# Kernel tuning notes

Measured on AMD Instinct MI355X. Metric: run time of the kernel, lower is better.

## Reference

```python
import jax, jax.numpy as jnp
import numpy as np

MAX_DISP = 4  # init kwarg


def setup_inputs() -> dict:
    key = jax.random.key(0)
    k1, k2 = jax.random.split(key)
    x_1 = jax.random.normal(k1, (8, 128, 128, 128), dtype=jnp.float32)
    x_2 = jax.random.normal(k2, (8, 128, 128, 128), dtype=jnp.float32)
    return {"x_1": x_1, "x_2": x_2}


def reference(x_1, x_2):
    d = MAX_DISP
    H, W = x_1.shape[2], x_1.shape[3]
    # zero-pad x_2 by max_disp on both spatial dims (ConstantPad2d)
    x2p = jnp.pad(x_2, ((0, 0), (0, 0), (d, d), (d, d)))
    # loop over the fixed (2d+1)^2 = 81 displacement offsets (structural, not data dim)
    outs = [
        jnp.mean(x_1 * x2p[:, :, dx:dx + H, dy:dy + W], axis=1)  # [B,H,W]
        for dx in range(2 * d + 1)
        for dy in range(2 * d + 1)
    ]
    return jnp.stack(outs, axis=1)  # [B, 81, H, W]
```

## Files before the change

kernel.cpp:

```cpp
#include <hip/hip_runtime.h>


constexpr int Cn = 128, Hn = 128, Wn = 128;
constexpr int HWn = Hn * Wn;
constexpr int TH = 4;
constexpr int NROWS = 16;
constexpr int ROWF  = 128;
constexpr int CHF   = NROWS * ROWF;
constexpr int BUFF  = 2 * CHF;

__device__ __forceinline__ float dpp_shr1(float x) {
  return __int_as_float(__builtin_amdgcn_update_dpp(
      0, __float_as_int(x), 0x111, 0xF, 0xF, true));
}
__device__ __forceinline__ float dpp_shl1(float x) {
  return __int_as_float(__builtin_amdgcn_update_dpp(
      0, __float_as_int(x), 0x101, 0xF, 0xF, true));
}

__global__ __launch_bounds__(576, 3)
void corr_kernel(const float* __restrict__ x1, const float* __restrict__ x2,
                 float* __restrict__ out) {
  __shared__ float lds[2][2][NROWS][ROWF];

  const int t    = threadIdx.x;
  const int w    = t >> 6;
  const int lane = t & 63;
  const int r    = lane >> 4;
  const int l    = lane & 15;

  const int phys = blockIdx.x;
  const int b    = phys & 7;
  const int tile = phys >> 3;
  const int h0   = tile * TH;
  const int dh   = w - 4;

  const bool stg  = t < 512;
  const int ridx  = t >> 5;
  const int s     = t & 31;
  const int j     = (s < 16) ? (s << 1) : (((s - 16) << 1) | 1);
  int gr;
  bool okg;
  if (ridx < 4) { gr = h0 + ridx; okg = true; }
  else { gr = h0 + ridx - 8; okg = (unsigned)gr < (unsigned)Hn; }
  const float* src = (ridx < 4 ? x1 : x2) + (size_t)b * Cn * HWn
                   + (size_t)(okg ? gr : 0) * Wn + (j << 2);
  okg = okg && stg;
  float* const L = &lds[0][0][0][0];
  const int woff = ridx * ROWF + (s << 2);

  const int rx  = r + dh + 8;
  const int o1l = r * ROWF + (l << 2);
  const int o1h = o1l + 64;
  const int o2l = rx * ROWF + (l << 2);
  const int o2h = o2l + 64;

  float4 acc0[9], acc1[9];
#pragma unroll
  for (int dw = 0; dw < 9; ++dw) {
    acc0[dw] = make_float4(0.f, 0.f, 0.f, 0.f);
    acc1[dw] = make_float4(0.f, 0.f, 0.f, 0.f);
  }

  const float4 z4 = make_float4(0.f, 0.f, 0.f, 0.f);
  float4 pv0 = z4, pv1 = z4;
  if (okg) { pv0 = *(const float4*)src; pv1 = *(const float4*)(src + HWn); }
  src += 2 * HWn;

#pragma unroll 1
  for (int step = 0; step < 64; ++step) {
    const int bo = (step & 1) * BUFF;
    if (stg) {
      *(float4*)(L + bo + woff)       = pv0;
      *(float4*)(L + bo + CHF + woff) = pv1;
    }
    __syncthreads();
    if (okg && step < 63) {
      pv0 = *(const float4*)src;
      pv1 = *(const float4*)(src + HWn);
    }
    src += 2 * HWn;

#pragma unroll
    for (int ch = 0; ch < 2; ++ch) {
      const float* p = L + bo + ch * CHF;
      const float4 a0 = *(const float4*)(p + o1l);
      const float4 a1 = *(const float4*)(p + o1h);
      const float4 b0 = *(const float4*)(p + o2l);
      const float4 b1 = *(const float4*)(p + o2h);
      const float win[16] = {
          dpp_shr1(b1.x), dpp_shr1(b1.y), dpp_shr1(b1.z), dpp_shr1(b1.w),
          b0.x, b0.y, b0.z, b0.w,
          b1.x, b1.y, b1.z, b1.w,
          dpp_shl1(b0.x), dpp_shl1(b0.y), dpp_shl1(b0.z), dpp_shl1(b0.w)};
      const float av[8] = {a0.x, a0.y, a0.z, a0.w, a1.x, a1.y, a1.z, a1.w};
#pragma unroll
      for (int dw = 0; dw < 9; ++dw) {
        acc0[dw].x += av[0] * win[dw + 0];
        acc0[dw].y += av[1] * win[dw + 1];
        acc0[dw].z += av[2] * win[dw + 2];
        acc0[dw].w += av[3] * win[dw + 3];
        acc1[dw].x += av[4] * win[dw + 4];
        acc1[dw].y += av[5] * win[dw + 5];
        acc1[dw].z += av[6] * win[dw + 6];
        acc1[dw].w += av[7] * win[dw + 7];
      }
    }
  }

  const float scale = 1.0f / 128.0f;
  float* ob = out + ((size_t)b * 81 + (size_t)w * 9) * HWn
                  + (size_t)(h0 + r) * Wn + (l << 3);
#pragma unroll
  for (int dw = 0; dw < 9; ++dw) {
    float4 r0, r1;
    r0.x = acc0[dw].x * scale; r0.y = acc0[dw].y * scale;
    r0.z = acc0[dw].z * scale; r0.w = acc0[dw].w * scale;
    r1.x = acc1[dw].x * scale; r1.y = acc1[dw].y * scale;
    r1.z = acc1[dw].z * scale; r1.w = acc1[dw].w * scale;
    *(float4*)(ob + (size_t)dw * HWn)     = r0;
    *(float4*)(ob + (size_t)dw * HWn + 4) = r1;
  }
}

extern "C" void kernel_launch(void* const* d_in, const int* in_sizes, int n_in,
                              void* d_out, int out_size, void* d_ws, size_t ws_size,
                              hipStream_t stream) {
  const float* x1 = (const float*)d_in[0];
  const float* x2 = (const float*)d_in[1];
  float* out = (float*)d_out;
  const int n_wgs = 8 * (Hn / TH);
  corr_kernel<<<dim3(n_wgs), dim3(576), 0, stream>>>(x1, x2, out);
}
```

Measured before the change: 177.7 us.

## Halve row tile, use wavefront-wide DPP shifts, one float4 per lane

Shrinks the row tile from 4 to 2 rows, so each block stages 12 LDS rows instead of 16. Each lane now owns 4 contiguous output pixels (32 lanes per row) rather than 8, and neighbours come from wavefront-level DPP row shifts with explicit zeroing at the edges. Accumulator registers are halved, and the launch bounds ask for 5 blocks per CU to raise occupancy. In exchange, the grid doubles, the overlapping x2 halo rows are reloaded more often (more global traffic per output), and each LDS read feeds fewer FMAs.

```diff
diff --git a/kernel.cpp b/kernel.cpp
--- a/kernel.cpp
+++ b/kernel.cpp
@@ -3,22 +3,22 @@
 
 constexpr int Cn = 128, Hn = 128, Wn = 128;
 constexpr int HWn = Hn * Wn;
-constexpr int TH = 4;
-constexpr int NROWS = 16;
+constexpr int TH = 2;
+constexpr int NROWS = 12;
 constexpr int ROWF  = 128;
 constexpr int CHF   = NROWS * ROWF;
 constexpr int BUFF  = 2 * CHF;
 
-__device__ __forceinline__ float dpp_shr1(float x) {
+__device__ __forceinline__ float dpp_wshr1(float x) {
   return __int_as_float(__builtin_amdgcn_update_dpp(
-      0, __float_as_int(x), 0x111, 0xF, 0xF, true));
+      0, __float_as_int(x), 0x138, 0xF, 0xF, true));
 }
-__device__ __forceinline__ float dpp_shl1(float x) {
+__device__ __forceinline__ float dpp_wshl1(float x) {
   return __int_as_float(__builtin_amdgcn_update_dpp(
-      0, __float_as_int(x), 0x101, 0xF, 0xF, true));
+      0, __float_as_int(x), 0x130, 0xF, 0xF, true));
 }
 
-__global__ __launch_bounds__(576, 3)
+__global__ __launch_bounds__(576, 5)
 void corr_kernel(const float* __restrict__ x1, const float* __restrict__ x2,
                  float* __restrict__ out) {
   __shared__ float lds[2][2][NROWS][ROWF];
@@ -26,41 +26,36 @@
   const int t    = threadIdx.x;
   const int w    = t >> 6;
   const int lane = t & 63;
-  const int r    = lane >> 4;
-  const int l    = lane & 15;
+  const int r    = lane >> 5;
+  const int lh   = lane & 31;
 
   const int phys = blockIdx.x;
   const int b    = phys & 7;
   const int tile = phys >> 3;
   const int h0   = tile * TH;
-  const int dh   = w - 4;
 
-  const bool stg  = t < 512;
+  const bool stg  = t < 384;
   const int ridx  = t >> 5;
   const int s     = t & 31;
-  const int j     = (s < 16) ? (s << 1) : (((s - 16) << 1) | 1);
   int gr;
   bool okg;
-  if (ridx < 4) { gr = h0 + ridx; okg = true; }
-  else { gr = h0 + ridx - 8; okg = (unsigned)gr < (unsigned)Hn; }
-  const float* src = (ridx < 4 ? x1 : x2) + (size_t)b * Cn * HWn
-                   + (size_t)(okg ? gr : 0) * Wn + (j << 2);
+  if (ridx < 2) { gr = h0 + ridx; okg = true; }
+  else { gr = h0 + ridx - 6; okg = (unsigned)gr < (unsigned)Hn; }
   okg = okg && stg;
+  const float* src = (ridx < 2 ? x1 : x2) + (size_t)b * Cn * HWn
+                   + (size_t)(okg ? gr : 0) * Wn + (s << 2);
   float* const L = &lds[0][0][0][0];
-  const int woff = ridx * ROWF + (s << 2);
+  const int woff = t << 2;
 
-  const int rx  = r + dh + 8;
-  const int o1l = r * ROWF + (l << 2);
-  const int o1h = o1l + 64;
-  const int o2l = rx * ROWF + (l << 2);
-  const int o2h = o2l + 64;
+  const int o1 = r * ROWF + (lh << 2);
+  const int o2 = (r + w + 2) * ROWF + (lh << 2);
 
-  float4 acc0[9], acc1[9];
+  const bool lEdge = (lh == 0);
+  const bool rEdge = (lh == 31);
+
+  float4 acc[9];
 #pragma unroll
-  for (int dw = 0; dw < 9; ++dw) {
-    acc0[dw] = make_float4(0.f, 0.f, 0.f, 0.f);
-    acc1[dw] = make_float4(0.f, 0.f, 0.f, 0.f);
-  }
+  for (int dw = 0; dw < 9; ++dw) acc[dw] = make_float4(0.f, 0.f, 0.f, 0.f);
 
   const float4 z4 = make_float4(0.f, 0.f, 0.f, 0.f);
   float4 pv0 = z4, pv1 = z4;
@@ -84,42 +79,36 @@
 #pragma unroll
     for (int ch = 0; ch < 2; ++ch) {
       const float* p = L + bo + ch * CHF;
-      const float4 a0 = *(const float4*)(p + o1l);
-      const float4 a1 = *(const float4*)(p + o1h);
-      const float4 b0 = *(const float4*)(p + o2l);
-      const float4 b1 = *(const float4*)(p + o2h);
-      const float win[16] = {
-          dpp_shr1(b1.x), dpp_shr1(b1.y), dpp_shr1(b1.z), dpp_shr1(b1.w),
-          b0.x, b0.y, b0.z, b0.w,
-          b1.x, b1.y, b1.z, b1.w,
-          dpp_shl1(b0.x), dpp_shl1(b0.y), dpp_shl1(b0.z), dpp_shl1(b0.w)};
-      const float av[8] = {a0.x, a0.y, a0.z, a0.w, a1.x, a1.y, a1.z, a1.w};
+      const float4 a  = *(const float4*)(p + o1);
+      const float4 b0 = *(const float4*)(p + o2);
+      float Lx = dpp_wshr1(b0.x), Ly = dpp_wshr1(b0.y),
+            Lz = dpp_wshr1(b0.z), Lw = dpp_wshr1(b0.w);
+      float Rx = dpp_wshl1(b0.x), Ry = dpp_wshl1(b0.y),
+            Rz = dpp_wshl1(b0.z), Rw = dpp_wshl1(b0.w);
+      if (lEdge) { Lx = 0.f; Ly = 0.f; Lz = 0.f; Lw = 0.f; }
+      if (rEdge) { Rx = 0.f; Ry = 0.f; Rz = 0.f; Rw = 0.f; }
+      const float win[12] = {Lx, Ly, Lz, Lw,
+                             b0.x, b0.y, b0.z, b0.w,
+                             Rx, Ry, Rz, Rw};
 #pragma unroll
       for (int dw = 0; dw < 9; ++dw) {
-        acc0[dw].x += av[0] * win[dw + 0];
-        acc0[dw].y += av[1] * win[dw + 1];
-        acc0[dw].z += av[2] * win[dw + 2];
-        acc0[dw].w += av[3] * win[dw + 3];
-        acc1[dw].x += av[4] * win[dw + 4];
-        acc1[dw].y += av[5] * win[dw + 5];
-        acc1[dw].z += av[6] * win[dw + 6];
-        acc1[dw].w += av[7] * win[dw + 7];
+        acc[dw].x += a.x * win[dw + 0];
+        acc[dw].y += a.y * win[dw + 1];
+        acc[dw].z += a.z * win[dw + 2];
+        acc[dw].w += a.w * win[dw + 3];
       }
     }
   }
 
   const float scale = 1.0f / 128.0f;
   float* ob = out + ((size_t)b * 81 + (size_t)w * 9) * HWn
-                  + (size_t)(h0 + r) * Wn + (l << 3);
+                  + (size_t)(h0 + r) * Wn + (lh << 2);
 #pragma unroll
   for (int dw = 0; dw < 9; ++dw) {
-    float4 r0, r1;
-    r0.x = acc0[dw].x * scale; r0.y = acc0[dw].y * scale;
-    r0.z = acc0[dw].z * scale; r0.w = acc0[dw].w * scale;
-    r1.x = acc1[dw].x * scale; r1.y = acc1[dw].y * scale;
-    r1.z = acc1[dw].z * scale; r1.w = acc1[dw].w * scale;
-    *(float4*)(ob + (size_t)dw * HWn)     = r0;
-    *(float4*)(ob + (size_t)dw * HWn + 4) = r1;
+    float4 rz;
+    rz.x = acc[dw].x * scale; rz.y = acc[dw].y * scale;
+    rz.z = acc[dw].z * scale; rz.w = acc[dw].w * scale;
+    *(float4*)(ob + (size_t)dw * HWn) = rz;
   }
 }
 
```

New measurement: 182.1 us. +2.4%, slower.

## Read x1 directly from global and stage four x2 channels per barrier

Applied to the files above, without the earlier changes.

x1 is no longer staged through LDS. Each thread now loads its x1 values straight from global memory, and LDS holds only the 12 padded x2 rows. Each barrier step now covers 4 channels instead of 2, which halves the number of __syncthreads calls and frees staging threads. The cost is a larger LDS footprint, x1 loads issued by all 9 waves and served from cache, and x1 global load latency that now sits inside the compute loop without explicit prefetch.

```diff
diff --git a/kernel.cpp b/kernel.cpp
--- a/kernel.cpp
+++ b/kernel.cpp
@@ -4,10 +4,11 @@
 constexpr int Cn = 128, Hn = 128, Wn = 128;
 constexpr int HWn = Hn * Wn;
 constexpr int TH = 4;
-constexpr int NROWS = 16;
-constexpr int ROWF  = 128;
-constexpr int CHF   = NROWS * ROWF;
-constexpr int BUFF  = 2 * CHF;
+constexpr int NR2  = 12;
+constexpr int ROWF = 128;
+constexpr int CHF  = NR2 * ROWF;
+constexpr int SLAB = 4;
+constexpr int BUFF = SLAB * CHF;
 
 __device__ __forceinline__ float dpp_shr1(float x) {
   return __int_as_float(__builtin_amdgcn_update_dpp(
@@ -21,7 +22,7 @@
 __global__ __launch_bounds__(576, 3)
 void corr_kernel(const float* __restrict__ x1, const float* __restrict__ x2,
                  float* __restrict__ out) {
-  __shared__ float lds[2][2][NROWS][ROWF];
+  __shared__ float lds[2][SLAB][NR2][ROWF];
 
   const int t    = threadIdx.x;
   const int w    = t >> 6;
@@ -33,27 +34,22 @@
   const int b    = phys & 7;
   const int tile = phys >> 3;
   const int h0   = tile * TH;
-  const int dh   = w - 4;
 
-  const bool stg  = t < 512;
-  const int ridx  = t >> 5;
-  const int s     = t & 31;
-  const int j     = (s < 16) ? (s << 1) : (((s - 16) << 1) | 1);
-  int gr;
-  bool okg;
-  if (ridx < 4) { gr = h0 + ridx; okg = true; }
-  else { gr = h0 + ridx - 8; okg = (unsigned)gr < (unsigned)Hn; }
-  const float* src = (ridx < 4 ? x1 : x2) + (size_t)b * Cn * HWn
+  const bool stg = t < 384;
+  const int ridx = t >> 5;
+  const int s    = t & 31;
+  const int j    = (s < 16) ? (s << 1) : (((s - 16) << 1) | 1);
+  const int gr   = h0 + ridx - 4;
+  const bool okg = stg && ((unsigned)gr < (unsigned)Hn);
+  const float* src = x2 + (size_t)b * Cn * HWn
                    + (size_t)(okg ? gr : 0) * Wn + (j << 2);
-  okg = okg && stg;
   float* const L = &lds[0][0][0][0];
-  const int woff = ridx * ROWF + (s << 2);
+  const int woff = t << 2;
 
-  const int rx  = r + dh + 8;
-  const int o1l = r * ROWF + (l << 2);
-  const int o1h = o1l + 64;
-  const int o2l = rx * ROWF + (l << 2);
+  const int o2l = (r + w) * ROWF + (l << 2);
   const int o2h = o2l + 64;
+  const float* p1 = x1 + (size_t)b * Cn * HWn
+                  + (size_t)(h0 + r) * Wn + (l << 3);
 
   float4 acc0[9], acc1[9];
 #pragma unroll
@@ -63,29 +59,39 @@
   }
 
   const float4 z4 = make_float4(0.f, 0.f, 0.f, 0.f);
-  float4 pv0 = z4, pv1 = z4;
-  if (okg) { pv0 = *(const float4*)src; pv1 = *(const float4*)(src + HWn); }
-  src += 2 * HWn;
+  float4 pv0 = z4, pv1 = z4, pv2 = z4, pv3 = z4;
+  if (okg) {
+    pv0 = *(const float4*)src;
+    pv1 = *(const float4*)(src + HWn);
+    pv2 = *(const float4*)(src + 2 * HWn);
+    pv3 = *(const float4*)(src + 3 * HWn);
+  }
+  src += (size_t)SLAB * HWn;
 
 #pragma unroll 1
-  for (int step = 0; step < 64; ++step) {
+  for (int step = 0; step < Cn / SLAB; ++step) {
     const int bo = (step & 1) * BUFF;
     if (stg) {
-      *(float4*)(L + bo + woff)       = pv0;
-      *(float4*)(L + bo + CHF + woff) = pv1;
+      *(float4*)(L + bo + woff)           = pv0;
+      *(float4*)(L + bo + CHF + woff)     = pv1;
+      *(float4*)(L + bo + 2 * CHF + woff) = pv2;
+      *(float4*)(L + bo + 3 * CHF + woff) = pv3;
     }
     __syncthreads();
-    if (okg && step < 63) {
+    if (okg && step < Cn / SLAB - 1) {
       pv0 = *(const float4*)src;
       pv1 = *(const float4*)(src + HWn);
+      pv2 = *(const float4*)(src + 2 * HWn);
+      pv3 = *(const float4*)(src + 3 * HWn);
     }
-    src += 2 * HWn;
+    src += (size_t)SLAB * HWn;
 
 #pragma unroll
-    for (int ch = 0; ch < 2; ++ch) {
-      const float* p = L + bo + ch * CHF;
-      const float4 a0 = *(const float4*)(p + o1l);
-      const float4 a1 = *(const float4*)(p + o1h);
+    for (int sc = 0; sc < SLAB; ++sc) {
+      const float* p = L + bo + sc * CHF;
+      const float* pc1 = p1 + (size_t)(step * SLAB + sc) * HWn;
+      const float4 a0 = *(const float4*)(pc1);
+      const float4 a1 = *(const float4*)(pc1 + 4);
       const float4 b0 = *(const float4*)(p + o2l);
       const float4 b1 = *(const float4*)(p + o2h);
       const float win[16] = {
```

After: 249.4 us. 1.4x slower.

## Deepen global prefetch to two stages and use raw barrier with lgkm wait

Applied to the files above, without the earlier changes.

Prefetches four channels ahead into two register sets and unrolls the main loop by two so each LDS buffer has a fixed offset. The __syncthreads is replaced with an explicit lgkmcnt wait plus s_barrier, so outstanding global loads are not forced to drain at the barrier. The aim is more memory latency hiding per barrier, at the cost of extra registers (eight more VGPRs for staging) under the 576-thread, 3-block launch bound.

```diff
diff --git a/kernel.cpp b/kernel.cpp
--- a/kernel.cpp
+++ b/kernel.cpp
@@ -33,12 +33,11 @@
   const int b    = phys & 7;
   const int tile = phys >> 3;
   const int h0   = tile * TH;
-  const int dh   = w - 4;
 
-  const bool stg  = t < 512;
-  const int ridx  = t >> 5;
-  const int s     = t & 31;
-  const int j     = (s < 16) ? (s << 1) : (((s - 16) << 1) | 1);
+  const bool stg = t < 512;
+  const int ridx = t >> 5;
+  const int s    = t & 31;
+  const int j    = (s < 16) ? (s << 1) : (((s - 16) << 1) | 1);
   int gr;
   bool okg;
   if (ridx < 4) { gr = h0 + ridx; okg = true; }
@@ -49,7 +48,7 @@
   float* const L = &lds[0][0][0][0];
   const int woff = ridx * ROWF + (s << 2);
 
-  const int rx  = r + dh + 8;
+  const int rx  = r + w + 4;
   const int o1l = r * ROWF + (l << 2);
   const int o1h = o1l + 64;
   const int o2l = rx * ROWF + (l << 2);
@@ -62,51 +61,65 @@
     acc1[dw] = make_float4(0.f, 0.f, 0.f, 0.f);
   }
 
+  auto compute_ch = [&](const float* p) {
+    const float4 a0 = *(const float4*)(p + o1l);
+    const float4 a1 = *(const float4*)(p + o1h);
+    const float4 b0 = *(const float4*)(p + o2l);
+    const float4 b1 = *(const float4*)(p + o2h);
+    const float win[16] = {
+        dpp_shr1(b1.x), dpp_shr1(b1.y), dpp_shr1(b1.z), dpp_shr1(b1.w),
+        b0.x, b0.y, b0.z, b0.w,
+        b1.x, b1.y, b1.z, b1.w,
+        dpp_shl1(b0.x), dpp_shl1(b0.y), dpp_shl1(b0.z), dpp_shl1(b0.w)};
+    const float av[8] = {a0.x, a0.y, a0.z, a0.w, a1.x, a1.y, a1.z, a1.w};
+#pragma unroll
+    for (int dw = 0; dw < 9; ++dw) {
+      acc0[dw].x += av[0] * win[dw + 0];
+      acc0[dw].y += av[1] * win[dw + 1];
+      acc0[dw].z += av[2] * win[dw + 2];
+      acc0[dw].w += av[3] * win[dw + 3];
+      acc1[dw].x += av[4] * win[dw + 4];
+      acc1[dw].y += av[5] * win[dw + 5];
+      acc1[dw].z += av[6] * win[dw + 6];
+      acc1[dw].w += av[7] * win[dw + 7];
+    }
+  };
+
   const float4 z4 = make_float4(0.f, 0.f, 0.f, 0.f);
-  float4 pv0 = z4, pv1 = z4;
-  if (okg) { pv0 = *(const float4*)src; pv1 = *(const float4*)(src + HWn); }
-  src += 2 * HWn;
+  float4 svA0 = z4, svA1 = z4, svB0 = z4, svB1 = z4;
+  if (okg) {
+    svA0 = *(const float4*)src;
+    svA1 = *(const float4*)(src + HWn);
+    svB0 = *(const float4*)(src + 2 * (size_t)HWn);
+    svB1 = *(const float4*)(src + 3 * (size_t)HWn);
+  }
+  src += 4 * (size_t)HWn;
+
+#define SUBITER(SV0, SV1, BO, GUARD)                                   \
+  do {                                                                 \
+    if (stg) {                                                         \
+      *(float4*)(L + (BO) + woff)       = SV0;                         \
+      *(float4*)(L + (BO) + CHF + woff) = SV1;                         \
+    }                                                                  \
+    asm volatile("s_waitcnt lgkmcnt(0)" ::: "memory");                 \
+    __builtin_amdgcn_s_barrier();                                      \
+    asm volatile("" ::: "memory");                                     \
+    if (okg && (GUARD)) {                                              \
+      SV0 = *(const float4*)src;                                       \
+      SV1 = *(const float4*)(src + HWn);                               \
+    }                                                                  \
+    src += 2 * (size_t)HWn;                                            \
+    compute_ch(L + (BO));                                              \
+    compute_ch(L + (BO) + CHF);                                        \
+  } while (0)
 
 #pragma unroll 1
-  for (int step = 0; step < 64; ++step) {
-    const int bo = (step & 1) * BUFF;
-    if (stg) {
-      *(float4*)(L + bo + woff)       = pv0;
-      *(float4*)(L + bo + CHF + woff) = pv1;
-    }
-    __syncthreads();
-    if (okg && step < 63) {
-      pv0 = *(const float4*)src;
-      pv1 = *(const float4*)(src + HWn);
-    }
-    src += 2 * HWn;
-
-#pragma unroll
-    for (int ch = 0; ch < 2; ++ch) {
-      const float* p = L + bo + ch * CHF;
-      const float4 a0 = *(const float4*)(p + o1l);
-      const float4 a1 = *(const float4*)(p + o1h);
-      const float4 b0 = *(const float4*)(p + o2l);
-      const float4 b1 = *(const float4*)(p + o2h);
-      const float win[16] = {
-          dpp_shr1(b1.x), dpp_shr1(b1.y), dpp_shr1(b1.z), dpp_shr1(b1.w),
-          b0.x, b0.y, b0.z, b0.w,
-          b1.x, b1.y, b1.z, b1.w,
-          dpp_shl1(b0.x), dpp_shl1(b0.y), dpp_shl1(b0.z), dpp_shl1(b0.w)};
-      const float av[8] = {a0.x, a0.y, a0.z, a0.w, a1.x, a1.y, a1.z, a1.w};
-#pragma unroll
-      for (int dw = 0; dw < 9; ++dw) {
-        acc0[dw].x += av[0] * win[dw + 0];
-        acc0[dw].y += av[1] * win[dw + 1];
-        acc0[dw].z += av[2] * win[dw + 2];
-        acc0[dw].w += av[3] * win[dw + 3];
-        acc1[dw].x += av[4] * win[dw + 4];
-        acc1[dw].y += av[5] * win[dw + 5];
-        acc1[dw].z += av[6] * win[dw + 6];
-        acc1[dw].w += av[7] * win[dw + 7];
-      }
-    }
+  for (int sp = 0; sp < 32; ++sp) {
+    const bool gu = sp < 31;
+    SUBITER(svA0, svA1, 0, gu);
+    SUBITER(svB0, svB1, BUFF, gu);
   }
+#undef SUBITER
 
   const float scale = 1.0f / 128.0f;
   float* ob = out + ((size_t)b * 81 + (size_t)w * 9) * HWn
```

After: 187.2 us. 5.3% more time.
